# Performance work log

Hardware: AMD Instinct MI355X
Metric: run time of the kernel (lower is better)

The kernel has to match this reference:

```python
import jax, jax.numpy as jnp
import numpy as np

# Body-part joint index groups (NTU-25 layout), as in the torch module
TORSO = np.array([0, 1, 2, 3, 20])
LEFT_HAND = np.array([8, 9, 10, 11, 23, 24])
LEFT_LEG = np.array([16, 17, 18, 19])
RIGHT_HAND = np.array([4, 5, 6, 7, 21, 22])
RIGHT_LEG = np.array([12, 13, 14, 15])
GROUPS = [TORSO, LEFT_HAND, LEFT_LEG, RIGHT_HAND, RIGHT_LEG]

N, C, T, V = 64, 256, 64, 25
HID = C // 16


def setup_inputs() -> dict:
    key = jax.random.key(0)
    k = jax.random.split(key, 5)
    x = jax.random.normal(k[0], (N, C, T, V), dtype=jnp.float32)
    # 5 branch MLPs (1x1 convs == linear over channels), stacked on leading axis f
    W1s = jax.random.normal(k[1], (5, HID, C), dtype=jnp.float32) * (1.0 / np.sqrt(C))
    b1s = jax.random.normal(k[2], (5, HID), dtype=jnp.float32) * 0.01
    W2s = jax.random.normal(k[3], (5, C, HID), dtype=jnp.float32) * (1.0 / np.sqrt(HID))
    b2s = jax.random.normal(k[4], (5, C), dtype=jnp.float32) * 0.01
    return {"x": x, "W1s": W1s, "b1s": b1s, "W2s": W2s, "b2s": b2s}


def _branch_mlp(p, W1s, b1s, W2s, b2s):
    # p: [N, C] pooled features; apply all 5 branch MLPs at once -> [N, 5, C]
    h = jax.nn.relu(jnp.einsum("nc,fhc->nfh", p, W1s) + b1s[None])  # [N,5,HID]
    return jnp.einsum("nfh,fch->nfc", h, W2s) + b2s[None]  # [N,5,C]


def reference(x, W1s, b1s, W2s, b2s):
    torso = x[:, :, :, TORSO]  # [N,C,T,5]
    avg = jnp.mean(torso, axis=(2, 3))  # [N,C] (AdaptiveAvgPool2d(1))
    mx = jnp.max(torso, axis=(2, 3))  # [N,C] (AdaptiveMaxPool2d(1))
    gates = jax.nn.sigmoid(_branch_mlp(avg, W1s, b1s, W2s, b2s)
                           + _branch_mlp(mx, W1s, b1s, W2s, b2s))  # [N,5,C]
    parts = [x[:, :, :, idx] * gates[:, i][:, :, None, None]
             for i, idx in enumerate(GROUPS)]
    return jnp.concatenate(parts, axis=3)  # [N,C,T,25]
```

## Files before the change

kernel.cpp:

```cpp
#include <hip/hip_runtime.h>
#include <math.h>

#define NB    64
#define CC    256
#define TT    64
#define VV    25
#define HID   16
#define NG    5
#define ROWF  1600
#define ROWF4 400
#define PAIRS 4

#define TORSO_MASK 0x10000Fu

__constant__ int SRC_J[25] = {0,1,2,3,20,  8,9,10,11,23,24,  16,17,18,19,  4,5,6,7,21,22,  12,13,14,15};
__constant__ int GRP_J[25] = {0,0,0,0,0,   1,1,1,1,1,1,      2,2,2,2,      3,3,3,3,3,3,   4,4,4,4};

__global__ void pool_kernel(const float4* __restrict__ x4,
                            float* __restrict__ avg_out,
                            float* __restrict__ max_out) {
    const int wave = threadIdx.x >> 6;
    const int lane = threadIdx.x & 63;
    const int pair = blockIdx.x * 4 + wave;
    const int base4 = pair * ROWF4;

    float s = 0.0f;
    float m = -3.4e38f;
    for (int i = lane; i < ROWF4; i += 64) {
        float4 v = x4[base4 + i];
        const int e = 4 * i;
        int j = e % 25;
        float vals[4] = {v.x, v.y, v.z, v.w};
        #pragma unroll
        for (int k = 0; k < 4; ++k) {
            int jj = j + k;
            if (jj >= 25) jj -= 25;
            if ((TORSO_MASK >> jj) & 1u) {
                s += vals[k];
                m = fmaxf(m, vals[k]);
            }
        }
    }
    #pragma unroll
    for (int off = 32; off >= 1; off >>= 1) {
        s += __shfl_xor(s, off, 64);
        m = fmaxf(m, __shfl_xor(m, off, 64));
    }
    if (lane == 0) {
        avg_out[pair] = s * (1.0f / (TT * 5));
        max_out[pair] = m;
    }
}

__global__ void gates_kernel(const float* __restrict__ avg_in,
                             const float* __restrict__ max_in,
                             const float* __restrict__ W1s,
                             const float* __restrict__ b1s,
                             const float* __restrict__ W2s,
                             const float* __restrict__ b2s,
                             float* __restrict__ gates) {
    __shared__ float4 sAvg[CC / 4];
    __shared__ float4 sMax[CC / 4];
    __shared__ float sHA[NG * HID];
    __shared__ float sHM[NG * HID];

    const int n = blockIdx.x;
    const int tid = threadIdx.x;

    if (tid < 64)       sAvg[tid]      = reinterpret_cast<const float4*>(avg_in + n * CC)[tid];
    else if (tid < 128) sMax[tid - 64] = reinterpret_cast<const float4*>(max_in + n * CC)[tid - 64];
    __syncthreads();

    if (tid < 2 * NG * HID) {
        const int type = tid / (NG * HID);
        const int rem  = tid % (NG * HID);
        const float4* p = type ? sMax : sAvg;
        const float4* w = reinterpret_cast<const float4*>(W1s + rem * CC);
        float h = b1s[rem];
        #pragma unroll 8
        for (int c4 = 0; c4 < CC / 4; ++c4) {
            float4 a = w[c4], b = p[c4];
            h += a.x * b.x + a.y * b.y + a.z * b.z + a.w * b.w;
        }
        h = fmaxf(h, 0.0f);
        if (type) sHM[rem] = h; else sHA[rem] = h;
    }
    __syncthreads();

    const int c = tid;
    #pragma unroll
    for (int f = 0; f < NG; ++f) {
        const float4* w2 = reinterpret_cast<const float4*>(W2s + (f * CC + c) * HID);
        float g = 2.0f * b2s[f * CC + c];
        #pragma unroll
        for (int j4 = 0; j4 < HID / 4; ++j4) {
            float4 w = w2[j4];
            const int jb = f * HID + j4 * 4;
            g += w.x * (sHA[jb + 0] + sHM[jb + 0]);
            g += w.y * (sHA[jb + 1] + sHM[jb + 1]);
            g += w.z * (sHA[jb + 2] + sHM[jb + 2]);
            g += w.w * (sHA[jb + 3] + sHM[jb + 3]);
        }
        gates[(n * NG + f) * CC + c] = 1.0f / (1.0f + expf(-g));
    }
}

__global__ void apply_kernel(const float4* __restrict__ x4,
                             const float* __restrict__ gates,
                             float4* __restrict__ out4) {
    __shared__ __align__(16) float xt[PAIRS * ROWF];
    __shared__ uint2 sLut4[VV];

    const int tid  = threadIdx.x;
    const int b    = blockIdx.x;
    const int w    = tid >> 6;
    const int lane = tid & 63;
    const int base4 = b * PAIRS * ROWF4;

    #pragma unroll
    for (int i = tid; i < PAIRS * ROWF4; i += 256) {
        reinterpret_cast<float4*>(xt)[i] = x4[base4 + i];
    }

    if (tid < VV) {
        unsigned lo = 0, hi = 0;
        #pragma unroll
        for (int j = 0; j < 4; ++j) {
            const int pp   = tid + j;
            const int wrap = (pp >= VV) ? 1 : 0;
            const int pm   = pp - VV * wrap;
            const unsigned e = (unsigned)(SRC_J[pm] + VV * wrap) | ((unsigned)GRP_J[pm] << 8);
            if (j < 2) lo |= e << (16 * j);
            else       hi |= e << (16 * (j - 2));
        }
        sLut4[tid] = make_uint2(lo, hi);
    }

    const int pair = b * PAIRS + w;
    const int n = pair >> 8;
    const int c = pair & (CC - 1);
    const float g0 = gates[(n * NG + 0) * CC + c];
    const float g1 = gates[(n * NG + 1) * CC + c];
    const float g2 = gates[(n * NG + 2) * CC + c];
    const float g3 = gates[(n * NG + 3) * CC + c];
    const float g4 = gates[(n * NG + 4) * CC + c];

    __syncthreads();

    const float* lrow = xt + w * ROWF;
    #pragma unroll
    for (int k = 0; k < 7; ++k) {
        const int il = 64 * k + lane;
        if (il < ROWF4) {
            const int e0   = 4 * il;
            const int row0 = e0 / VV;
            const int p0   = e0 - row0 * VV;
            const uint2 lut = sLut4[p0];
            float r[4];
            #pragma unroll
            for (int j = 0; j < 4; ++j) {
                const unsigned half   = ((j < 2) ? lut.x : lut.y) >> (16 * (j & 1));
                const unsigned srcoff = half & 63u;
                const unsigned grp    = (half >> 8) & 7u;
                float gt = g0;
                gt = (grp >= 1u) ? g1 : gt;
                gt = (grp >= 2u) ? g2 : gt;
                gt = (grp >= 3u) ? g3 : gt;
                gt = (grp >= 4u) ? g4 : gt;
                r[j] = lrow[row0 * VV + (int)srcoff] * gt;
            }
            out4[base4 + w * ROWF4 + il] = make_float4(r[0], r[1], r[2], r[3]);
        }
    }
}

extern "C" void kernel_launch(void* const* d_in, const int* in_sizes, int n_in,
                              void* d_out, int out_size, void* d_ws, size_t ws_size,
                              hipStream_t stream) {
    const float* x   = (const float*)d_in[0];
    const float* W1s = (const float*)d_in[1];
    const float* b1s = (const float*)d_in[2];
    const float* W2s = (const float*)d_in[3];
    const float* b2s = (const float*)d_in[4];

    float* avg   = (float*)d_ws;
    float* mx    = avg + NB * CC;
    float* gates = mx + NB * CC;

    pool_kernel<<<(NB * CC) / 4, 256, 0, stream>>>(
        (const float4*)x, avg, mx);

    gates_kernel<<<NB, CC, 0, stream>>>(avg, mx, W1s, b1s, W2s, b2s, gates);

    apply_kernel<<<(NB * CC) / PAIRS, 256, 0, stream>>>(
        (const float4*)x, gates, (float4*)d_out);
}
```

Before: 219.7 us.

## Fuse pool, gate MLP and apply into one kernel with per-sample grid barrier

Measured after the change: 296.2 us. 34.8% more time.

```diff
diff --git a/kernel.cpp b/kernel.cpp
--- a/kernel.cpp
+++ b/kernel.cpp
@@ -1,126 +1,56 @@
 #include <hip/hip_runtime.h>
 #include <math.h>
 
-#define NB    64
-#define CC    256
-#define TT    64
-#define VV    25
-#define HID   16
-#define NG    5
-#define ROWF  1600
-#define ROWF4 400
-#define PAIRS 4
+#define NB     64
+#define CC     256
+#define TT     64
+#define VV     25
+#define HID    16
+#define NG     5
+#define ROWF   1600
+#define ROWF4  400
+#define PAIRS  4
+#define CHUNKS 4
+#define BPG    16
+#define NBLK   (NB * BPG)
 
 #define TORSO_MASK 0x10000Fu
 
 __constant__ int SRC_J[25] = {0,1,2,3,20,  8,9,10,11,23,24,  16,17,18,19,  4,5,6,7,21,22,  12,13,14,15};
 __constant__ int GRP_J[25] = {0,0,0,0,0,   1,1,1,1,1,1,      2,2,2,2,      3,3,3,3,3,3,   4,4,4,4};
 
-__global__ void pool_kernel(const float4* __restrict__ x4,
-                            float* __restrict__ avg_out,
-                            float* __restrict__ max_out) {
-    const int wave = threadIdx.x >> 6;
-    const int lane = threadIdx.x & 63;
-    const int pair = blockIdx.x * 4 + wave;
-    const int base4 = pair * ROWF4;
-
-    float s = 0.0f;
-    float m = -3.4e38f;
-    for (int i = lane; i < ROWF4; i += 64) {
-        float4 v = x4[base4 + i];
-        const int e = 4 * i;
-        int j = e % 25;
-        float vals[4] = {v.x, v.y, v.z, v.w};
-        #pragma unroll
-        for (int k = 0; k < 4; ++k) {
-            int jj = j + k;
-            if (jj >= 25) jj -= 25;
-            if ((TORSO_MASK >> jj) & 1u) {
-                s += vals[k];
-                m = fmaxf(m, vals[k]);
-            }
-        }
-    }
-    #pragma unroll
-    for (int off = 32; off >= 1; off >>= 1) {
-        s += __shfl_xor(s, off, 64);
-        m = fmaxf(m, __shfl_xor(m, off, 64));
-    }
-    if (lane == 0) {
-        avg_out[pair] = s * (1.0f / (TT * 5));
-        max_out[pair] = m;
-    }
-}
-
-__global__ void gates_kernel(const float* __restrict__ avg_in,
-                             const float* __restrict__ max_in,
-                             const float* __restrict__ W1s,
-                             const float* __restrict__ b1s,
-                             const float* __restrict__ W2s,
-                             const float* __restrict__ b2s,
-                             float* __restrict__ gates) {
-    __shared__ float4 sAvg[CC / 4];
-    __shared__ float4 sMax[CC / 4];
+__device__ inline void st_agent(float* p, float v) {
+    __hip_atomic_store(p, v, __ATOMIC_RELAXED, __HIP_MEMORY_SCOPE_AGENT);
+}
+__device__ inline float ld_agent(const float* p) {
+    return __hip_atomic_load(p, __ATOMIC_RELAXED, __HIP_MEMORY_SCOPE_AGENT);
+}
+
+__global__ __launch_bounds__(256, 4)
+void fused_kernel(const float4* __restrict__ x4,
+                  const float* __restrict__ W1s,
+                  const float* __restrict__ b1s,
+                  const float* __restrict__ W2s,
+                  const float* __restrict__ b2s,
+                  float4* __restrict__ out4,
+                  float* __restrict__ ws_avg,
+                  float* __restrict__ ws_max,
+                  unsigned* __restrict__ cnt) {
+    __shared__ __align__(16) float xt[PAIRS * ROWF];
+    __shared__ __align__(16) float sAvg[CC];
+    __shared__ __align__(16) float sMax[CC];
     __shared__ float sHA[NG * HID];
     __shared__ float sHM[NG * HID];
-
-    const int n = blockIdx.x;
-    const int tid = threadIdx.x;
-
-    if (tid < 64)       sAvg[tid]      = reinterpret_cast<const float4*>(avg_in + n * CC)[tid];
-    else if (tid < 128) sMax[tid - 64] = reinterpret_cast<const float4*>(max_in + n * CC)[tid - 64];
-    __syncthreads();
-
-    if (tid < 2 * NG * HID) {
-        const int type = tid / (NG * HID);
-        const int rem  = tid % (NG * HID);
-        const float4* p = type ? sMax : sAvg;
-        const float4* w = reinterpret_cast<const float4*>(W1s + rem * CC);
-        float h = b1s[rem];
-        #pragma unroll 8
-        for (int c4 = 0; c4 < CC / 4; ++c4) {
-            float4 a = w[c4], b = p[c4];
-            h += a.x * b.x + a.y * b.y + a.z * b.z + a.w * b.w;
-        }
-        h = fmaxf(h, 0.0f);
-        if (type) sHM[rem] = h; else sHA[rem] = h;
-    }
-    __syncthreads();
-
-    const int c = tid;
-    #pragma unroll
-    for (int f = 0; f < NG; ++f) {
-        const float4* w2 = reinterpret_cast<const float4*>(W2s + (f * CC + c) * HID);
-        float g = 2.0f * b2s[f * CC + c];
-        #pragma unroll
-        for (int j4 = 0; j4 < HID / 4; ++j4) {
-            float4 w = w2[j4];
-            const int jb = f * HID + j4 * 4;
-            g += w.x * (sHA[jb + 0] + sHM[jb + 0]);
-            g += w.y * (sHA[jb + 1] + sHM[jb + 1]);
-            g += w.z * (sHA[jb + 2] + sHM[jb + 2]);
-            g += w.w * (sHA[jb + 3] + sHM[jb + 3]);
-        }
-        gates[(n * NG + f) * CC + c] = 1.0f / (1.0f + expf(-g));
-    }
-}
-
-__global__ void apply_kernel(const float4* __restrict__ x4,
-                             const float* __restrict__ gates,
-                             float4* __restrict__ out4) {
-    __shared__ __align__(16) float xt[PAIRS * ROWF];
+    __shared__ float sg[CHUNKS * PAIRS * NG];
     __shared__ uint2 sLut4[VV];
 
     const int tid  = threadIdx.x;
     const int b    = blockIdx.x;
     const int w    = tid >> 6;
     const int lane = tid & 63;
-    const int base4 = b * PAIRS * ROWF4;
-
-    #pragma unroll
-    for (int i = tid; i < PAIRS * ROWF4; i += 256) {
-        reinterpret_cast<float4*>(xt)[i] = x4[base4 + i];
-    }
+    const int n    = b >> 4;
+    const int sub  = b & 15;
+    const int pairbase = n * CC + sub * (CHUNKS * PAIRS);
 
     if (tid < VV) {
         unsigned lo = 0, hi = 0;
@@ -136,40 +66,132 @@
         sLut4[tid] = make_uint2(lo, hi);
     }
 
-    const int pair = b * PAIRS + w;
-    const int n = pair >> 8;
-    const int c = pair & (CC - 1);
-    const float g0 = gates[(n * NG + 0) * CC + c];
-    const float g1 = gates[(n * NG + 1) * CC + c];
-    const float g2 = gates[(n * NG + 2) * CC + c];
-    const float g3 = gates[(n * NG + 3) * CC + c];
-    const float g4 = gates[(n * NG + 4) * CC + c];
-
-    __syncthreads();
-
-    const float* lrow = xt + w * ROWF;
     #pragma unroll
-    for (int k = 0; k < 7; ++k) {
-        const int il = 64 * k + lane;
-        if (il < ROWF4) {
-            const int e0   = 4 * il;
-            const int row0 = e0 / VV;
-            const int p0   = e0 - row0 * VV;
-            const uint2 lut = sLut4[p0];
-            float r[4];
+    for (int ch = 0; ch < CHUNKS; ++ch) {
+        const int pair  = pairbase + ch * PAIRS + w;
+        const int base4 = pair * ROWF4;
+        float4* xtw = reinterpret_cast<float4*>(xt + w * ROWF);
+        float s = 0.0f;
+        float m = -3.4e38f;
+        for (int i = lane; i < ROWF4; i += 64) {
+            float4 v = x4[base4 + i];
+            if (ch == CHUNKS - 1) xtw[i] = v;
+            const int e = 4 * i;
+            int j = e % 25;
+            float vals[4] = {v.x, v.y, v.z, v.w};
             #pragma unroll
-            for (int j = 0; j < 4; ++j) {
-                const unsigned half   = ((j < 2) ? lut.x : lut.y) >> (16 * (j & 1));
-                const unsigned srcoff = half & 63u;
-                const unsigned grp    = (half >> 8) & 7u;
-                float gt = g0;
-                gt = (grp >= 1u) ? g1 : gt;
-                gt = (grp >= 2u) ? g2 : gt;
-                gt = (grp >= 3u) ? g3 : gt;
-                gt = (grp >= 4u) ? g4 : gt;
-                r[j] = lrow[row0 * VV + (int)srcoff] * gt;
+            for (int k = 0; k < 4; ++k) {
+                int jj = j + k;
+                if (jj >= 25) jj -= 25;
+                if ((TORSO_MASK >> jj) & 1u) {
+                    s += vals[k];
+                    m = fmaxf(m, vals[k]);
+                }
             }
-            out4[base4 + w * ROWF4 + il] = make_float4(r[0], r[1], r[2], r[3]);
+        }
+        #pragma unroll
+        for (int off = 32; off >= 1; off >>= 1) {
+            s += __shfl_xor(s, off, 64);
+            m = fmaxf(m, __shfl_xor(m, off, 64));
+        }
+        if (lane == 0) {
+            st_agent(ws_avg + pair, s * (1.0f / (TT * 5)));
+            st_agent(ws_max + pair, m);
+        }
+    }
+
+    __syncthreads();
+    if (tid == 0) {
+        __hip_atomic_fetch_add(cnt + n, 1u, __ATOMIC_RELEASE, __HIP_MEMORY_SCOPE_AGENT);
+        while (__hip_atomic_load(cnt + n, __ATOMIC_ACQUIRE, __HIP_MEMORY_SCOPE_AGENT) < BPG) {
+            __builtin_amdgcn_s_sleep(8);
+        }
+    }
+    __syncthreads();
+
+    sAvg[tid] = ld_agent(ws_avg + n * CC + tid);
+    sMax[tid] = ld_agent(ws_max + n * CC + tid);
+    __syncthreads();
+
+    if (tid < 2 * NG * HID) {
+        const int type = tid / (NG * HID);
+        const int rem  = tid % (NG * HID);
+        const float4* p  = reinterpret_cast<const float4*>(type ? sMax : sAvg);
+        const float4* wv = reinterpret_cast<const float4*>(W1s + rem * CC);
+        float h = b1s[rem];
+        #pragma unroll 8
+        for (int c4 = 0; c4 < CC / 4; ++c4) {
+            float4 a = wv[c4], q = p[c4];
+            h += a.x * q.x + a.y * q.y + a.z * q.z + a.w * q.w;
+        }
+        h = fmaxf(h, 0.0f);
+        if (type) sHM[rem] = h; else sHA[rem] = h;
+    }
+    __syncthreads();
+
+    if (tid < CHUNKS * PAIRS * NG) {
+        const int lp = tid / NG;
+        const int f  = tid % NG;
+        const int cch = (pairbase + lp) & (CC - 1);
+        const float4* w2 = reinterpret_cast<const float4*>(W2s + (f * CC + cch) * HID);
+        float g = 2.0f * b2s[f * CC + cch];
+        #pragma unroll
+        for (int j4 = 0; j4 < HID / 4; ++j4) {
+            float4 wq = w2[j4];
+            const int jb = f * HID + j4 * 4;
+            g += wq.x * (sHA[jb + 0] + sHM[jb + 0]);
+            g += wq.y * (sHA[jb + 1] + sHM[jb + 1]);
+            g += wq.z * (sHA[jb + 2] + sHM[jb + 2]);
+            g += wq.w * (sHA[jb + 3] + sHM[jb + 3]);
+        }
+        sg[tid] = 1.0f / (1.0f + expf(-g));
+    }
+    __syncthreads();
+
+    #pragma unroll
+    for (int step = 0; step < CHUNKS; ++step) {
+        const int ch = (step == 0) ? (CHUNKS - 1) : (step - 1);
+        const int pair  = pairbase + ch * PAIRS + w;
+        const int base4 = pair * ROWF4;
+        float4* xtw = reinterpret_cast<float4*>(xt + w * ROWF);
+
+        if (step != 0) {
+            __syncthreads();
+            for (int i = lane; i < ROWF4; i += 64) xtw[i] = x4[base4 + i];
+            __syncthreads();
+        }
+
+        const int gbase = (ch * PAIRS + w) * NG;
+        const float g0 = sg[gbase + 0];
+        const float g1 = sg[gbase + 1];
+        const float g2 = sg[gbase + 2];
+        const float g3 = sg[gbase + 3];
+        const float g4 = sg[gbase + 4];
+
+        const float* lrow = xt + w * ROWF;
+        #pragma unroll
+        for (int k = 0; k < 7; ++k) {
+            const int il = 64 * k + lane;
+            if (il < ROWF4) {
+                const int e0   = 4 * il;
+                const int row0 = e0 / VV;
+                const int p0   = e0 - row0 * VV;
+                const uint2 lut = sLut4[p0];
+                float r[4];
+                #pragma unroll
+                for (int j = 0; j < 4; ++j) {
+                    const unsigned half   = ((j < 2) ? lut.x : lut.y) >> (16 * (j & 1));
+                    const unsigned srcoff = half & 63u;
+                    const unsigned grp    = (half >> 8) & 7u;
+                    float gt = g0;
+                    gt = (grp >= 1u) ? g1 : gt;
+                    gt = (grp >= 2u) ? g2 : gt;
+                    gt = (grp >= 3u) ? g3 : gt;
+                    gt = (grp >= 4u) ? g4 : gt;
+                    r[j] = lrow[row0 * VV + (int)srcoff] * gt;
+                }
+                out4[base4 + il] = make_float4(r[0], r[1], r[2], r[3]);
+            }
         }
     }
 }
@@ -183,15 +205,14 @@
     const float* W2s = (const float*)d_in[3];
     const float* b2s = (const float*)d_in[4];
 
-    float* avg   = (float*)d_ws;
-    float* mx    = avg + NB * CC;
-    float* gates = mx + NB * CC;
-
-    pool_kernel<<<(NB * CC) / 4, 256, 0, stream>>>(
-        (const float4*)x, avg, mx);
-
-    gates_kernel<<<NB, CC, 0, stream>>>(avg, mx, W1s, b1s, W2s, b2s, gates);
-
-    apply_kernel<<<(NB * CC) / PAIRS, 256, 0, stream>>>(
-        (const float4*)x, gates, (float4*)d_out);
-}
+    float* avg = (float*)d_ws;
+    float* mx  = avg + NB * CC;
+    size_t cnt_off = ((size_t)(NB * CC * 2) * 4 + 255) & ~(size_t)255;
+    unsigned* cnt = (unsigned*)((char*)d_ws + cnt_off);
+
+    hipMemsetAsync(cnt, 0, NB * sizeof(unsigned), stream);
+
+    fused_kernel<<<NBLK, 256, 0, stream>>>(
+        (const float4*)x, W1s, b1s, W2s, b2s,
+        (float4*)d_out, avg, mx, cnt);
+}
```
